# Performance work log

Hardware: AMD Instinct MI355X
Metric: run time of the kernel (lower is better)

The kernel has to match this reference:

```python
import jax, jax.numpy as jnp
import numpy as np

B_SZ, L, H, P = 16, 1024, 256, 256
DT_MIN, DT_MAX = 1e-3, 1e-1


def setup_inputs() -> dict:
    key = jax.random.key(0)
    ks = jax.random.split(key, 6)
    u = jax.random.normal(ks[0], (B_SZ, L, H), dtype=jnp.float32)
    # Stable diagonal init (stands in for HiPPO-LegS diag: negative real part,
    # spread imaginary parts) so exp(Lambda*Delta) has |.|<1 over long scans.
    Lambda_re = -0.5 * jnp.ones((P,), jnp.float32)
    Lambda_im = jnp.pi * jnp.arange(P, dtype=jnp.float32)
    Bp = jax.random.normal(ks[1], (P, H, 2), jnp.float32) / jnp.sqrt(2.0 * H)  # (P,H,2) real/imag
    Cp = jax.random.normal(ks[2], (H, P, 2), jnp.float32) / jnp.sqrt(2.0 * P)  # (H,P,2) real/imag
    D = jax.random.normal(ks[3], (H,), jnp.float32)
    log_step = (jax.random.uniform(ks[4], (P, 1), jnp.float32)
                * (jnp.log(DT_MAX) - jnp.log(DT_MIN)) + jnp.log(DT_MIN))
    return {"u": u, "Lambda_re": Lambda_re, "Lambda_im": Lambda_im,
            "B": Bp, "C": Cp, "D": D, "log_step": log_step}


def _binop(ei, ej):
    # S5 associative scan element: (A, Bu); compose linear recurrences.
    ai, bi = ei
    aj, bj = ej
    return aj * ai, aj * bi + bj


def reference(u, Lambda_re, Lambda_im, B, C, D, log_step):
    # clip_eigs=False, step_rescale=1.0, conj_sym=True, discretization='zoh'
    Lambda = Lambda_re + 1j * Lambda_im                     # (P,) complex
    B_tilde = B[..., 0] + 1j * B[..., 1]                    # (P,H) complex
    C_tilde = C[..., 0] + 1j * C[..., 1]                    # (H,P) complex
    Delta = jnp.exp(log_step[:, 0])                         # (P,)
    # ZOH discretization
    Lambda_bar = jnp.exp(Lambda * Delta)                    # (P,)
    B_bar = ((Lambda_bar - 1.0) / Lambda)[:, None] * B_tilde  # (P,H)
    # Input projection: (B, L, P) complex
    Bu = jnp.einsum('ph,blh->blp', B_bar, u.astype(B_bar.dtype))
    Lam = jnp.broadcast_to(Lambda_bar, Bu.shape)            # (B, L, P)
    # Parallel associative scan over time axis
    _, xs = jax.lax.associative_scan(_binop, (Lam, Bu), axis=1)  # states (B,L,P)
    # Output projection; conj_sym -> 2 * real part
    ys = 2.0 * jnp.einsum('hp,blp->blh', C_tilde, xs).real  # (B,L,H)
    return ys + D * u                                       # feedthrough
```

## Files before the change

kernel.cpp:

```cpp
#include <hip/hip_runtime.h>
#include <hip/hip_bf16.h>
#include <math.h>

#define BB     16
#define LSEQ   1024
#define HH     256
#define PP     256
#define LC     32
#define NC     (LSEQ/LC)
#define NCHUNK (BB*NC)

#define OFF_W1T  0u
#define OFF_W2T  262144u
#define OFF_PW   524288u
#define OFF_CEND 655360u
#define OFF_BAR  2752512u

typedef __attribute__((ext_vector_type(8))) short short8;
typedef __attribute__((ext_vector_type(4))) float floatx4;
typedef unsigned long long ull;

__device__ __forceinline__ float bf2f(unsigned hs) {
    union { unsigned u; float f; } v; v.u = hs << 16; return v.f;
}
__device__ __forceinline__ unsigned short f2bs(float f) {
    __hip_bfloat16 h = __float2bfloat16(f);
    union { __hip_bfloat16 h; unsigned short s; } v; v.h = h; return v.s;
}
__device__ __forceinline__ unsigned packbf(float r, float i) {
    return (unsigned)f2bs(r) | ((unsigned)f2bs(i) << 16);
}
__device__ __forceinline__ float2 lam_pow(float lr, float li, float dtt) {
    float m = expf(lr * dtt);
    return make_float2(m * cosf(li * dtt), m * sinf(li * dtt));
}
__device__ __forceinline__ void cohst32(unsigned* p, unsigned v) {
    __hip_atomic_store(p, v, __ATOMIC_RELAXED, __HIP_MEMORY_SCOPE_AGENT);
}
__device__ __forceinline__ void cohst64(ull* p, float2 v) {
    ull b; __builtin_memcpy(&b, &v, 8);
    __hip_atomic_store(p, b, __ATOMIC_RELAXED, __HIP_MEMORY_SCOPE_AGENT);
}

__device__ __forceinline__ void treebar(char* base, int inst) {
    asm volatile("s_waitcnt vmcnt(0)" ::: "memory");
    __syncthreads();
    if (threadIdx.x == 0) {
        char* b = base + inst * 8192;
        const unsigned g = blockIdx.x >> 4;
        unsigned* gcnt  = (unsigned*)(b + g * 64);
        unsigned* gflag = (unsigned*)(b + 2048 + g * 64);
        unsigned* rcnt  = (unsigned*)(b + 4096);
        unsigned* rflag = (unsigned*)(b + 4160);
        unsigned r = __hip_atomic_fetch_add(gcnt, 1u, __ATOMIC_RELAXED,
                                            __HIP_MEMORY_SCOPE_AGENT);
        if (r == 15) {
            unsigned rr = __hip_atomic_fetch_add(rcnt, 1u, __ATOMIC_RELAXED,
                                                 __HIP_MEMORY_SCOPE_AGENT);
            if (rr == 31) {
                __hip_atomic_store(rflag, 1u, __ATOMIC_RELAXED, __HIP_MEMORY_SCOPE_AGENT);
            } else {
                for (int it = 0; it < (1 << 18); ++it) {
                    if (__hip_atomic_load(rflag, __ATOMIC_RELAXED, __HIP_MEMORY_SCOPE_AGENT))
                        break;
                    __builtin_amdgcn_s_sleep(4);
                }
            }
            __hip_atomic_store(gflag, 1u, __ATOMIC_RELAXED, __HIP_MEMORY_SCOPE_AGENT);
        } else {
            for (int it = 0; it < (1 << 18); ++it) {
                if (__hip_atomic_load(gflag, __ATOMIC_RELAXED, __HIP_MEMORY_SCOPE_AGENT))
                    break;
                __builtin_amdgcn_s_sleep(4);
            }
        }
    }
    __syncthreads();
}

#define XSTRS 520
#define XSTRD 260
#define CARR_OFF 33280

__global__ __launch_bounds__(512, 4) void k_all(
        const float* __restrict__ u, const float* __restrict__ Lr,
        const float* __restrict__ Li, const float* __restrict__ ls,
        const float* __restrict__ Bm, const float* __restrict__ Cm,
        const float* __restrict__ D, float* __restrict__ out,
        char* __restrict__ ws) {
    extern __shared__ char smem[];
    char* barbase = ws + OFF_BAR;

    const int tid = threadIdx.x, bc = blockIdx.x;
    const int wave = tid >> 6, lane = tid & 63;
    const int q = lane >> 4, rr = lane & 15;
    const int m0 = bc * LC;

    const int arow = tid >> 4, acol = (tid & 15) * 16;
    float4 uv[4];
    {
        const float* up = u + (size_t)(m0 + arow) * 256 + acol;
        #pragma unroll
        for (int i = 0; i < 4; ++i) uv[i] = *(const float4*)(up + 4 * i);
    }

    if (bc < 256) {
        if (tid < 128) {
            int p = bc, t = tid;
            float lr = Lr[p], li = Li[p];
            float dt = expf(ls[p]);
            float2 lam = lam_pow(lr, li, dt);
            float den = lr * lr + li * li;
            float nr = lam.x - 1.0f, ni = lam.y;
            float cr = (nr * lr + ni * li) / den;
            float ci = (ni * lr - nr * li) / den;
            float4 bv = *(const float4*)(Bm + (size_t)p * 512 + 4 * t);
            unsigned rev = packbf(cr * bv.x - ci * bv.y, cr * bv.z - ci * bv.w);
            unsigned imv = packbf(cr * bv.y + ci * bv.x, cr * bv.w + ci * bv.z);
            unsigned* w1u = (unsigned*)(ws + OFF_W1T);
            cohst32(&w1u[(2 * p) * 128 + t], rev);
            cohst32(&w1u[(2 * p + 1) * 128 + t], imv);
            if (t <= 32)
                cohst64((ull*)(ws + OFF_PW) + (size_t)t * 256 + p,
                        lam_pow(lr, li, dt * (float)t));
        }
    } else {
        if (tid < 256) {
            int h = bc - 256, p = tid;
            float c_r = Cm[(h * PP + p) * 2 + 0];
            float c_i = Cm[(h * PP + p) * 2 + 1];
            cohst32((unsigned*)(ws + OFF_W2T) + h * 256 + p, packbf(2.0f * c_r, -2.0f * c_i));
        }
    }

    {
        unsigned pk[8];
        #pragma unroll
        for (int i = 0; i < 4; ++i) {
            pk[2 * i]     = packbf(uv[i].x, uv[i].y);
            pk[2 * i + 1] = packbf(uv[i].z, uv[i].w);
        }
        const int kb = acol * 2;
        const int msk = (arow & 7) << 4;
        char* A = smem;
        *(uint4*)(A + arow * 512 + (kb ^ msk))        = make_uint4(pk[0], pk[1], pk[2], pk[3]);
        *(uint4*)(A + arow * 512 + ((kb + 16) ^ msk)) = make_uint4(pk[4], pk[5], pk[6], pk[7]);
    }
    treebar(barbase, 0);

    {
        const char* W1 = (const char*)(ws + OFF_W1T);
        const char* A = smem;
        const int amask = (rr & 7) << 4;
        floatx4 acc[2][4];
        #pragma unroll
        for (int i = 0; i < 2; ++i)
            #pragma unroll
            for (int j = 0; j < 4; ++j) acc[i][j] = (floatx4)0.0f;

        #pragma unroll 2
        for (int hs = 0; hs < 8; ++hs) {
            const int kb = hs * 64 + q * 16;
            short8 a0 = *(const short8*)(A + rr * 512 + (kb ^ amask));
            short8 a1 = *(const short8*)(A + (16 + rr) * 512 + (kb ^ amask));
            #pragma unroll
            for (int j = 0; j < 4; ++j) {
                short8 b = *(const short8*)(W1 + (size_t)(wave * 64 + j * 16 + rr) * 512 + kb);
                acc[0][j] = __builtin_amdgcn_mfma_f32_16x16x32_bf16(a0, b, acc[0][j], 0, 0, 0);
                acc[1][j] = __builtin_amdgcn_mfma_f32_16x16x32_bf16(a1, b, acc[1][j], 0, 0, 0);
            }
        }
        __syncthreads();
        unsigned short* X = (unsigned short*)smem;
        #pragma unroll
        for (int i = 0; i < 2; ++i)
            #pragma unroll
            for (int j = 0; j < 4; ++j)
                #pragma unroll
                for (int r0 = 0; r0 < 4; ++r0)
                    X[(i * 16 + q * 4 + r0) * XSTRS + wave * 64 + j * 16 + rr] =
                        f2bs(acc[i][j][r0]);
        __syncthreads();
    }

    if (tid < 256) {
        const int pq = tid;
        const float2 lam = lam_pow(Lr[pq], Li[pq], expf(ls[pq]));
        unsigned* X32 = (unsigned*)smem;
        float xr = 0.0f, xi = 0.0f;
        #pragma unroll
        for (int j = 0; j < LC; ++j) {
            unsigned cv = X32[j * XSTRD + pq];
            float br = bf2f(cv & 0xffffu), bi = bf2f(cv >> 16);
            float nr = fmaf(lam.x, xr, fmaf(-lam.y, xi, br));
            float ni = fmaf(lam.x, xi, fmaf(lam.y, xr, bi));
            xr = nr; xi = ni;
            X32[j * XSTRD + pq] = packbf(xr, xi);
        }
        cohst64((ull*)(ws + OFF_CEND) + (size_t)bc * 256 + pq, make_float2(xr, xi));
    }
    treebar(barbase, 1);

    {
        float2* carrs = (float2*)(smem + CARR_OFF);
        if (tid < 256) {
            const int p = tid;
            const int c = bc & (NC - 1);
            const int b0 = bc & ~(NC - 1);
            const float2* cend = (const float2*)(ws + OFF_CEND);
            const float2 g = lam_pow(Lr[p], Li[p], expf(ls[p]) * (float)LC);
            float sr = 0.0f, si = 0.0f;
            float gpr = 1.0f, gpi = 0.0f;
            #pragma unroll
            for (int k = 0; k < NC - 1; ++k) {
                int idx = c - 1 - k; idx = idx < 0 ? 0 : idx;
                float2 e = cend[(size_t)(b0 + idx) * 256 + p];
                float er = (k < c) ? e.x : 0.0f;
                float ei = (k < c) ? e.y : 0.0f;
                sr = fmaf(gpr, er, fmaf(-gpi, ei, sr));
                si = fmaf(gpr, ei, fmaf(gpi, er, si));
                float t2 = gpr * g.x - gpi * g.y;
                gpi = gpr * g.y + gpi * g.x; gpr = t2;
            }
            carrs[p] = make_float2(sr, si);
        }
        __syncthreads();
    }

    {
        float2* carrs = (float2*)(smem + CARR_OFF);
        unsigned* X32 = (unsigned*)smem;
        const float2* pw = (const float2*)(ws + OFF_PW);
        const int frow = tid >> 4, fcol = tid & 15;
        const float2* pwr = pw + (size_t)(frow + 1) * 256;
        #pragma unroll 4
        for (int e = 0; e < 16; ++e) {
            int p = fcol + e * 16;
            unsigned cv = X32[frow * XSTRD + p];
            float2 pwv = pwr[p];
            float2 cav = carrs[p];
            float fr = pwv.x * cav.x - pwv.y * cav.y;
            float fi = pwv.x * cav.y + pwv.y * cav.x;
            X32[frow * XSTRD + p] =
                packbf(bf2f(cv & 0xffffu) + fr, bf2f(cv >> 16) + fi);
        }
        __syncthreads();
    }

    {
        const char* W2 = (const char*)(ws + OFF_W2T);
        const char* Xb = (const char*)smem;
        floatx4 acc[2][2];
        #pragma unroll
        for (int i = 0; i < 2; ++i)
            #pragma unroll
            for (int j = 0; j < 2; ++j) acc[i][j] = (floatx4)0.0f;

        #pragma unroll 2
        for (int hs = 0; hs < 16; ++hs) {
            const int kb = hs * 64 + q * 16;
            short8 a[2], bfr[2];
            #pragma unroll
            for (int i = 0; i < 2; ++i)
                a[i] = *(const short8*)(Xb + (i * 16 + rr) * (XSTRS * 2) + kb);
            #pragma unroll
            for (int j = 0; j < 2; ++j)
                bfr[j] = *(const short8*)(W2 + (size_t)(wave * 32 + j * 16 + rr) * 1024 + kb);
            #pragma unroll
            for (int i = 0; i < 2; ++i)
                #pragma unroll
                for (int j = 0; j < 2; ++j)
                    acc[i][j] = __builtin_amdgcn_mfma_f32_16x16x32_bf16(a[i], bfr[j], acc[i][j], 0, 0, 0);
        }

        #pragma unroll
        for (int i = 0; i < 2; ++i) {
            int mbase = m0 + i * 16 + q * 4;
            #pragma unroll
            for (int j = 0; j < 2; ++j) {
                int col = wave * 32 + j * 16 + rr;
                #pragma unroll
                for (int r0 = 0; r0 < 4; ++r0) {
                    int rw = mbase + r0;
                    size_t gi = (size_t)rw * 256 + col;
                    out[gi] = acc[i][j][r0] + D[col] * u[gi];
                }
            }
        }
    }
}

extern "C" void kernel_launch(void* const* d_in, const int* in_sizes, int n_in,
                              void* d_out, int out_size, void* d_ws, size_t ws_size,
                              hipStream_t stream) {
    const float* u  = (const float*)d_in[0];
    const float* Lr = (const float*)d_in[1];
    const float* Li = (const float*)d_in[2];
    const float* Bm = (const float*)d_in[3];
    const float* Cm = (const float*)d_in[4];
    const float* D  = (const float*)d_in[5];
    const float* ls = (const float*)d_in[6];
    float* out = (float*)d_out;
    char* ws = (char*)d_ws;

    hipMemsetAsync(ws + OFF_BAR, 0, 16384, stream);
    k_all<<<NCHUNK, 512, 35328, stream>>>(u, Lr, Li, ls, Bm, Cm, D, out, ws);
}
```

Before: 124.5 us.

## Split weight prep into separate kernel, stream weights via async LDS double buffering

Moves the B/C weight discretisation and power table into a separate prep kernel, which also zeroes the barrier area and replaces the memset. This removes the first grid-wide barrier from the main kernel. The two-level tree barrier becomes a per-batch barrier over 32 blocks. Both GEMMs now stage weight tiles into LDS with global_load_lds double buffering instead of reading global memory directly. LDS use grows from about 35 KB to 80 KB per block, which may lower occupancy, and the second launch adds its own overhead.

```diff
diff --git a/kernel.cpp b/kernel.cpp
--- a/kernel.cpp
+++ b/kernel.cpp
@@ -30,83 +30,48 @@
 __device__ __forceinline__ unsigned packbf(float r, float i) {
     return (unsigned)f2bs(r) | ((unsigned)f2bs(i) << 16);
 }
+__device__ __forceinline__ void async16(const void* g, void* l) {
+    __builtin_amdgcn_global_load_lds(
+        (const __attribute__((address_space(1))) unsigned*)g,
+        (__attribute__((address_space(3))) unsigned*)l, 16, 0, 0);
+}
 __device__ __forceinline__ float2 lam_pow(float lr, float li, float dtt) {
     float m = expf(lr * dtt);
     return make_float2(m * cosf(li * dtt), m * sinf(li * dtt));
 }
-__device__ __forceinline__ void cohst32(unsigned* p, unsigned v) {
-    __hip_atomic_store(p, v, __ATOMIC_RELAXED, __HIP_MEMORY_SCOPE_AGENT);
-}
 __device__ __forceinline__ void cohst64(ull* p, float2 v) {
     ull b; __builtin_memcpy(&b, &v, 8);
     __hip_atomic_store(p, b, __ATOMIC_RELAXED, __HIP_MEMORY_SCOPE_AGENT);
 }
 
-__device__ __forceinline__ void treebar(char* base, int inst) {
+__device__ __forceinline__ void batchbar(char* base) {
     asm volatile("s_waitcnt vmcnt(0)" ::: "memory");
     __syncthreads();
     if (threadIdx.x == 0) {
-        char* b = base + inst * 8192;
-        const unsigned g = blockIdx.x >> 4;
-        unsigned* gcnt  = (unsigned*)(b + g * 64);
-        unsigned* gflag = (unsigned*)(b + 2048 + g * 64);
-        unsigned* rcnt  = (unsigned*)(b + 4096);
-        unsigned* rflag = (unsigned*)(b + 4160);
-        unsigned r = __hip_atomic_fetch_add(gcnt, 1u, __ATOMIC_RELAXED,
-                                            __HIP_MEMORY_SCOPE_AGENT);
-        if (r == 15) {
-            unsigned rr = __hip_atomic_fetch_add(rcnt, 1u, __ATOMIC_RELAXED,
-                                                 __HIP_MEMORY_SCOPE_AGENT);
-            if (rr == 31) {
-                __hip_atomic_store(rflag, 1u, __ATOMIC_RELAXED, __HIP_MEMORY_SCOPE_AGENT);
-            } else {
-                for (int it = 0; it < (1 << 18); ++it) {
-                    if (__hip_atomic_load(rflag, __ATOMIC_RELAXED, __HIP_MEMORY_SCOPE_AGENT))
-                        break;
-                    __builtin_amdgcn_s_sleep(4);
-                }
-            }
-            __hip_atomic_store(gflag, 1u, __ATOMIC_RELAXED, __HIP_MEMORY_SCOPE_AGENT);
+        const unsigned b = blockIdx.x >> 5;
+        unsigned* cnt  = (unsigned*)(base + b * 64);
+        unsigned* flag = (unsigned*)(base + 2048 + b * 64);
+        if (__hip_atomic_fetch_add(cnt, 1u, __ATOMIC_RELAXED,
+                                   __HIP_MEMORY_SCOPE_AGENT) == 31u) {
+            __hip_atomic_store(flag, 1u, __ATOMIC_RELAXED, __HIP_MEMORY_SCOPE_AGENT);
         } else {
             for (int it = 0; it < (1 << 18); ++it) {
-                if (__hip_atomic_load(gflag, __ATOMIC_RELAXED, __HIP_MEMORY_SCOPE_AGENT))
+                if (__hip_atomic_load(flag, __ATOMIC_RELAXED, __HIP_MEMORY_SCOPE_AGENT))
                     break;
-                __builtin_amdgcn_s_sleep(4);
+                __builtin_amdgcn_s_sleep(2);
             }
         }
     }
     __syncthreads();
 }
 
-#define XSTRS 520
-#define XSTRD 260
-#define CARR_OFF 33280
-
-__global__ __launch_bounds__(512, 4) void k_all(
-        const float* __restrict__ u, const float* __restrict__ Lr,
-        const float* __restrict__ Li, const float* __restrict__ ls,
-        const float* __restrict__ Bm, const float* __restrict__ Cm,
-        const float* __restrict__ D, float* __restrict__ out,
-        char* __restrict__ ws) {
-    extern __shared__ char smem[];
-    char* barbase = ws + OFF_BAR;
-
-    const int tid = threadIdx.x, bc = blockIdx.x;
-    const int wave = tid >> 6, lane = tid & 63;
-    const int q = lane >> 4, rr = lane & 15;
-    const int m0 = bc * LC;
-
-    const int arow = tid >> 4, acol = (tid & 15) * 16;
-    float4 uv[4];
-    {
-        const float* up = u + (size_t)(m0 + arow) * 256 + acol;
-        #pragma unroll
-        for (int i = 0; i < 4; ++i) uv[i] = *(const float4*)(up + 4 * i);
-    }
-
-    if (bc < 256) {
-        if (tid < 128) {
-            int p = bc, t = tid;
+__global__ void k_prep(const float* __restrict__ Bm, const float* __restrict__ Cm,
+                       const float* __restrict__ Lr, const float* __restrict__ Li,
+                       const float* __restrict__ ls, char* __restrict__ ws) {
+    int blk = blockIdx.x, t = threadIdx.x;
+    if (blk < 256) {
+        if (t < 128) {
+            int p = blk;
             float lr = Lr[p], li = Li[p];
             float dt = expf(ls[p]);
             float2 lam = lam_pow(lr, li, dt);
@@ -115,25 +80,58 @@
             float cr = (nr * lr + ni * li) / den;
             float ci = (ni * lr - nr * li) / den;
             float4 bv = *(const float4*)(Bm + (size_t)p * 512 + 4 * t);
-            unsigned rev = packbf(cr * bv.x - ci * bv.y, cr * bv.z - ci * bv.w);
-            unsigned imv = packbf(cr * bv.y + ci * bv.x, cr * bv.w + ci * bv.z);
             unsigned* w1u = (unsigned*)(ws + OFF_W1T);
-            cohst32(&w1u[(2 * p) * 128 + t], rev);
-            cohst32(&w1u[(2 * p + 1) * 128 + t], imv);
+            w1u[(2 * p) * 128 + t]     = packbf(cr * bv.x - ci * bv.y, cr * bv.z - ci * bv.w);
+            w1u[(2 * p + 1) * 128 + t] = packbf(cr * bv.y + ci * bv.x, cr * bv.w + ci * bv.z);
             if (t <= 32)
-                cohst64((ull*)(ws + OFF_PW) + (size_t)t * 256 + p,
-                        lam_pow(lr, li, dt * (float)t));
-        }
+                ((float2*)(ws + OFF_PW))[t * 256 + p] = lam_pow(lr, li, dt * (float)t);
+        }
+        if (blk == 0)
+            ((float4*)(ws + OFF_BAR))[t] = make_float4(0.f, 0.f, 0.f, 0.f);
     } else {
-        if (tid < 256) {
-            int h = bc - 256, p = tid;
-            float c_r = Cm[(h * PP + p) * 2 + 0];
-            float c_i = Cm[(h * PP + p) * 2 + 1];
-            cohst32((unsigned*)(ws + OFF_W2T) + h * 256 + p, packbf(2.0f * c_r, -2.0f * c_i));
-        }
-    }
-
-    {
+        int h = blk - 256, p = t;
+        float c_r = Cm[(h * PP + p) * 2 + 0];
+        float c_i = Cm[(h * PP + p) * 2 + 1];
+        ((unsigned*)(ws + OFF_W2T))[h * 256 + p] = packbf(2.0f * c_r, -2.0f * c_i);
+    }
+}
+
+#define XSTRS 520
+#define XSTRD 260
+#define CARR_OFF 33280
+#define B1_OFF  16384
+#define B2_OFF  35328
+
+__global__ __launch_bounds__(512, 4) void k_main(
+        const float* __restrict__ u, const float* __restrict__ Lr,
+        const float* __restrict__ Li, const float* __restrict__ ls,
+        const float* __restrict__ D, float* __restrict__ out,
+        char* __restrict__ ws) {
+    extern __shared__ char smem[];
+    const int tid = threadIdx.x, bc = blockIdx.x;
+    const int wave = tid >> 6, lane = tid & 63;
+    const int q = lane >> 4, rr = lane & 15;
+    const int m0 = bc * LC;
+    const int fs = (lane >> 3) & 3;
+    const int fr = (rr >> 1) & 3;
+
+    {
+        const char* W1 = (const char*)(ws + OFF_W1T);
+        char* dst = smem + B1_OFF + wave * 4096;
+        #pragma unroll
+        for (int i = 0; i < 4; ++i) {
+            int n = i * 64 + lane;
+            int R = wave * 64 + (n >> 2);
+            async16(W1 + (size_t)R * 512 + (((n & 3) ^ fs) << 4), dst + n * 16);
+        }
+    }
+
+    const int arow = tid >> 4, acol = (tid & 15) * 16;
+    {
+        float4 uv[4];
+        const float* up = u + (size_t)(m0 + arow) * 256 + acol;
+        #pragma unroll
+        for (int i = 0; i < 4; ++i) uv[i] = *(const float4*)(up + 4 * i);
         unsigned pk[8];
         #pragma unroll
         for (int i = 0; i < 4; ++i) {
@@ -146,7 +144,7 @@
         *(uint4*)(A + arow * 512 + (kb ^ msk))        = make_uint4(pk[0], pk[1], pk[2], pk[3]);
         *(uint4*)(A + arow * 512 + ((kb + 16) ^ msk)) = make_uint4(pk[4], pk[5], pk[6], pk[7]);
     }
-    treebar(barbase, 0);
+    __syncthreads();
 
     {
         const char* W1 = (const char*)(ws + OFF_W1T);
@@ -158,14 +156,25 @@
             #pragma unroll
             for (int j = 0; j < 4; ++j) acc[i][j] = (floatx4)0.0f;
 
-        #pragma unroll 2
-        for (int hs = 0; hs < 8; ++hs) {
-            const int kb = hs * 64 + q * 16;
-            short8 a0 = *(const short8*)(A + rr * 512 + (kb ^ amask));
-            short8 a1 = *(const short8*)(A + (16 + rr) * 512 + (kb ^ amask));
+        for (int t = 0; t < 8; ++t) {
+            asm volatile("s_waitcnt vmcnt(0)" ::: "memory");
+            if (t < 7) {
+                char* dst = smem + B1_OFF + ((t + 1) & 1) * 32768 + wave * 4096;
+                const char* src = W1 + (t + 1) * 64;
+                #pragma unroll
+                for (int i = 0; i < 4; ++i) {
+                    int n = i * 64 + lane;
+                    int R = wave * 64 + (n >> 2);
+                    async16(src + (size_t)R * 512 + (((n & 3) ^ fs) << 4), dst + n * 16);
+                }
+            }
+            const char* bb = smem + B1_OFF + (t & 1) * 32768 + wave * 4096;
+            const int kbA = t * 64 + q * 16;
+            short8 a0 = *(const short8*)(A + rr * 512 + (kbA ^ amask));
+            short8 a1 = *(const short8*)(A + (16 + rr) * 512 + (kbA ^ amask));
             #pragma unroll
             for (int j = 0; j < 4; ++j) {
-                short8 b = *(const short8*)(W1 + (size_t)(wave * 64 + j * 16 + rr) * 512 + kb);
+                short8 b = *(const short8*)(bb + (j * 16 + rr) * 64 + ((q ^ fr) << 4));
                 acc[0][j] = __builtin_amdgcn_mfma_f32_16x16x32_bf16(a0, b, acc[0][j], 0, 0, 0);
                 acc[1][j] = __builtin_amdgcn_mfma_f32_16x16x32_bf16(a1, b, acc[1][j], 0, 0, 0);
             }
@@ -198,8 +207,19 @@
             X32[j * XSTRD + pq] = packbf(xr, xi);
         }
         cohst64((ull*)(ws + OFF_CEND) + (size_t)bc * 256 + pq, make_float2(xr, xi));
-    }
-    treebar(barbase, 1);
+    } else {
+        const char* W2 = (const char*)(ws + OFF_W2T);
+        char* B2 = smem + B2_OFF;
+        const int t4 = tid - 256;
+        const int f0 = (t4 >> 3) & 3;
+        #pragma unroll
+        for (int i = 0; i < 4; ++i) {
+            int c = i * 256 + t4;
+            int R = c >> 2;
+            async16(W2 + (size_t)R * 1024 + (((c & 3) ^ f0) << 4), B2 + c * 16);
+        }
+    }
+    batchbar(ws + OFF_BAR);
 
     {
         float2* carrs = (float2*)(smem + CARR_OFF);
@@ -239,10 +259,10 @@
             unsigned cv = X32[frow * XSTRD + p];
             float2 pwv = pwr[p];
             float2 cav = carrs[p];
-            float fr = pwv.x * cav.x - pwv.y * cav.y;
-            float fi = pwv.x * cav.y + pwv.y * cav.x;
+            float fr2 = pwv.x * cav.x - pwv.y * cav.y;
+            float fi2 = pwv.x * cav.y + pwv.y * cav.x;
             X32[frow * XSTRD + p] =
-                packbf(bf2f(cv & 0xffffu) + fr, bf2f(cv >> 16) + fi);
+                packbf(bf2f(cv & 0xffffu) + fr2, bf2f(cv >> 16) + fi2);
         }
         __syncthreads();
     }
@@ -256,21 +276,28 @@
             #pragma unroll
             for (int j = 0; j < 2; ++j) acc[i][j] = (floatx4)0.0f;
 
-        #pragma unroll 2
-        for (int hs = 0; hs < 16; ++hs) {
-            const int kb = hs * 64 + q * 16;
-            short8 a[2], bfr[2];
-            #pragma unroll
-            for (int i = 0; i < 2; ++i)
-                a[i] = *(const short8*)(Xb + (i * 16 + rr) * (XSTRS * 2) + kb);
-            #pragma unroll
-            for (int j = 0; j < 2; ++j)
-                bfr[j] = *(const short8*)(W2 + (size_t)(wave * 32 + j * 16 + rr) * 1024 + kb);
-            #pragma unroll
-            for (int i = 0; i < 2; ++i)
+        for (int t = 0; t < 16; ++t) {
+            asm volatile("s_waitcnt vmcnt(0)" ::: "memory");
+            if (t < 15) {
+                char* dst = smem + B2_OFF + ((t + 1) & 1) * 16384 + wave * 2048;
+                const char* src = W2 + (t + 1) * 64;
                 #pragma unroll
-                for (int j = 0; j < 2; ++j)
-                    acc[i][j] = __builtin_amdgcn_mfma_f32_16x16x32_bf16(a[i], bfr[j], acc[i][j], 0, 0, 0);
+                for (int i = 0; i < 2; ++i) {
+                    int n = i * 64 + lane;
+                    int R = wave * 32 + (n >> 2);
+                    async16(src + (size_t)R * 1024 + (((n & 3) ^ fs) << 4), dst + n * 16);
+                }
+            }
+            const char* bbuf = smem + B2_OFF + (t & 1) * 16384 + wave * 2048;
+            const int kbA = t * 64 + q * 16;
+            short8 a0 = *(const short8*)(Xb + rr * (XSTRS * 2) + kbA);
+            short8 a1 = *(const short8*)(Xb + (16 + rr) * (XSTRS * 2) + kbA);
+            #pragma unroll
+            for (int j = 0; j < 2; ++j) {
+                short8 b = *(const short8*)(bbuf + (j * 16 + rr) * 64 + ((q ^ fr) << 4));
+                acc[0][j] = __builtin_amdgcn_mfma_f32_16x16x32_bf16(a0, b, acc[0][j], 0, 0, 0);
+                acc[1][j] = __builtin_amdgcn_mfma_f32_16x16x32_bf16(a1, b, acc[1][j], 0, 0, 0);
+            }
         }
 
         #pragma unroll
@@ -303,6 +330,6 @@
     float* out = (float*)d_out;
     char* ws = (char*)d_ws;
 
-    hipMemsetAsync(ws + OFF_BAR, 0, 16384, stream);
-    k_all<<<NCHUNK, 512, 35328, stream>>>(u, Lr, Li, ls, Bm, Cm, D, out, ws);
-}
+    k_prep<<<512, 256, 0, stream>>>(Bm, Cm, Lr, Li, ls, ws);
+    k_main<<<NCHUNK, 512, 81920, stream>>>(u, Lr, Li, ls, D, out, ws);
+}
```

New measurement: 104.0 us. 1.2x faster.
